# Performance work log

Measured on AMD Instinct MI355X. Metric: run time of the kernel, lower is better.

The kernel has to match this reference:

```python
import jax, jax.numpy as jnp
import numpy as np

EPS = 1e-3


def batchnorm(x, gamma, beta):
    # BatchNorm1d in training mode: batch mean and biased variance over dim 0
    mean = jnp.mean(x, axis=0)
    var = jnp.var(x, axis=0)  # biased, matches torch BN normalization
    return (x - mean) * jax.lax.rsqrt(var + EPS) * gamma + beta


def setup_inputs() -> dict:
    key = jax.random.key(0)
    ks = jax.random.split(key, 12)
    N, C_in, C_out, G = 400000, 64, 128, 30000
    points_xyz = jax.random.normal(ks[0], (N, 3), dtype=jnp.float32) * 10.0
    feat_all = jax.random.normal(ks[1], (N, C_in), dtype=jnp.float32)
    unq_inv = jax.random.randint(ks[2], (N,), 0, G, dtype=jnp.int32)
    s_in = 1.0 / np.sqrt(C_in)
    s3 = 1.0 / np.sqrt(3.0)
    return {
        "points_xyz": points_xyz,
        "feat_all": feat_all,
        "unq_inv": unq_inv,
        "W_pre": jax.random.uniform(ks[3], (C_in, C_out), jnp.float32, -s_in, s_in),
        "b_pre": jax.random.uniform(ks[4], (C_out,), jnp.float32, -s_in, s_in),
        "g1": jnp.ones((C_out,), jnp.float32),
        "be1": jnp.zeros((C_out,), jnp.float32),
        "Wp1": jax.random.uniform(ks[5], (3, C_out), jnp.float32, -s3, s3),
        "bp1": jax.random.uniform(ks[6], (C_out,), jnp.float32, -s3, s3),
        "Wp2": jax.random.uniform(ks[7], (3, C_out), jnp.float32, -s3, s3),
        "bp2": jax.random.uniform(ks[8], (C_out,), jnp.float32, -s3, s3),
        "g2": jnp.ones((C_out,), jnp.float32),
        "be2": jnp.zeros((C_out,), jnp.float32),
        "num_segments": 30000,
    }


def reference(points_xyz, feat_all, unq_inv, W_pre, b_pre, g1, be1,
              Wp1, bp1, Wp2, bp2, g2, be2, num_segments):
    p = jnp.floor(points_xyz)                       # [N, 3]
    feat = batchnorm(feat_all @ W_pre + b_pre, g1, be1)  # [N, C_out]
    pw1 = p @ Wp1 + bp1                             # [N, C_out]
    pw2 = p @ Wp2 + bp2                             # [N, C_out]
    feat_weight = pw1 * feat                        # [N, C_out]
    feat_add = jax.ops.segment_sum(feat_weight, unq_inv,
                                   num_segments=num_segments)  # [G, C_out]
    feat_add = feat_add[unq_inv]                    # gather back: [N, C_out]
    out = pw2 * feat - feat_add
    out = jax.nn.relu(batchnorm(out, g2, be2))
    return out
```

## Files before the change

kernel.cpp:

```cpp
#include <hip/hip_runtime.h>
#include <hip/hip_bf16.h>

typedef unsigned int u32;
typedef unsigned short u16;
typedef __attribute__((ext_vector_type(8))) short short8;
typedef __attribute__((ext_vector_type(4))) float floatx4;

#define COUT 128
#define GSEG 30000
#define BN_EPS 1e-3f

__device__ __forceinline__ u32 f2bf(float x) {
    u32 u = __float_as_uint(x);
    return (u + 0x7fffu + ((u >> 16) & 1u)) >> 16;
}
__device__ __forceinline__ float bf2f(u32 b) { return __uint_as_float(b << 16); }

__device__ __forceinline__ void unpack8(uint4 v, float* f) {
    f[0] = __uint_as_float(v.x << 16); f[1] = __uint_as_float(v.x & 0xffff0000u);
    f[2] = __uint_as_float(v.y << 16); f[3] = __uint_as_float(v.y & 0xffff0000u);
    f[4] = __uint_as_float(v.z << 16); f[5] = __uint_as_float(v.z & 0xffff0000u);
    f[6] = __uint_as_float(v.w << 16); f[7] = __uint_as_float(v.w & 0xffff0000u);
}

__global__ __launch_bounds__(512) void k_prep_w(
    const float* __restrict__ W, u16* __restrict__ wt_hi, u16* __restrict__ wt_lo)
{
    int t = threadIdx.x;
    for (int f = t; f < 8192; f += 512) {
        int k = f >> 7, c = f & 127;
        float w = W[f];
        u32 hb = f2bf(w);
        float lo = w - bf2f(hb);
        wt_hi[c * 64 + k] = (u16)hb;
        wt_lo[c * 64 + k] = (u16)f2bf(lo);
    }
}

__global__ __launch_bounds__(512) void k_gemm_bn1(
    const float* __restrict__ A, const u16* __restrict__ wt_hi, const u16* __restrict__ wt_lo,
    const float* __restrict__ bias, const int* __restrict__ unq, int* __restrict__ cnt,
    u16* __restrict__ lin, float* __restrict__ sum1, float* __restrict__ sumsq1, int n)
{
    __shared__ u16 pack[128 * 136];
    __shared__ float sSum[128], sSq[128];

    const int t = threadIdx.x;
    const int row0 = blockIdx.x * 128;
    if (t < 128) { sSum[t] = 0.f; sSq[t] = 0.f; }

    if (t < 128 && row0 + t < n) atomicAdd(&cnt[unq[row0 + t]], 1);

    const int lane = t & 63, wv = t >> 6;
    const int r = lane & 15, q = lane >> 4;
    const int rw0 = wv * 16;
    const int row_a = row0 + rw0 + r;
    const bool ok = row_a < n;

    short8 arh[2], arl[2];
    const float* ap = A + (size_t)row_a * 64;
#pragma unroll
    for (int ks = 0; ks < 2; ks++) {
        float4 v0 = make_float4(0.f, 0.f, 0.f, 0.f), v1 = v0;
        if (ok) {
            v0 = *(const float4*)(ap + ks * 32 + q * 8);
            v1 = *(const float4*)(ap + ks * 32 + q * 8 + 4);
        }
        float vv[8] = {v0.x, v0.y, v0.z, v0.w, v1.x, v1.y, v1.z, v1.w};
#pragma unroll
        for (int i = 0; i < 8; i++) {
            u32 hb = f2bf(vv[i]);
            float lo = vv[i] - bf2f(hb);
            arh[ks][i] = (short)(u16)hb;
            arl[ks][i] = (short)(u16)f2bf(lo);
        }
    }

    floatx4 acc[8];
#pragma unroll
    for (int ct = 0; ct < 8; ct++) acc[ct] = (floatx4){0.f, 0.f, 0.f, 0.f};

#pragma unroll
    for (int ct = 0; ct < 8; ct++) {
        const u16* whp = wt_hi + (ct * 16 + r) * 64 + q * 8;
        const u16* wlp = wt_lo + (ct * 16 + r) * 64 + q * 8;
#pragma unroll
        for (int ks = 0; ks < 2; ks++) {
            short8 wh = *(const short8*)(whp + ks * 32);
            short8 wl = *(const short8*)(wlp + ks * 32);
            acc[ct] = __builtin_amdgcn_mfma_f32_16x16x32_bf16(arh[ks], wh, acc[ct], 0, 0, 0);
            acc[ct] = __builtin_amdgcn_mfma_f32_16x16x32_bf16(arl[ks], wh, acc[ct], 0, 0, 0);
            acc[ct] = __builtin_amdgcn_mfma_f32_16x16x32_bf16(arh[ks], wl, acc[ct], 0, 0, 0);
        }
    }
    __syncthreads();

#pragma unroll
    for (int ct = 0; ct < 8; ct++) {
        int c = ct * 16 + r;
        float bv = bias[c];
        float ssum = 0.f, ssq = 0.f;
#pragma unroll
        for (int i = 0; i < 4; i++) {
            int lrow = rw0 + q * 4 + i;
            float v = acc[ct][i] + bv;
            if (row0 + lrow >= n) v = 0.f;
            ssum += v; ssq += v * v;
            pack[lrow * 136 + c] = (u16)f2bf(v);
        }
        ssum += __shfl_xor(ssum, 16, 64); ssq += __shfl_xor(ssq, 16, 64);
        ssum += __shfl_xor(ssum, 32, 64); ssq += __shfl_xor(ssq, 32, 64);
        if (lane < 16) { atomicAdd(&sSum[c], ssum); atomicAdd(&sSq[c], ssq); }
    }
    __syncthreads();

#pragma unroll
    for (int j = 0; j < 4; j++) {
        int f = t + j * 512;
        int row = f >> 4, c0 = (f & 15) << 3;
        if (row0 + row < n) {
            uint4 v = *(const uint4*)&pack[row * 136 + c0];
            *(uint4*)(lin + (size_t)(row0 + row) * 128 + c0) = v;
        }
    }
    if (t < 128) { atomicAdd(&sum1[t], sSum[t]); atomicAdd(&sumsq1[t], sSq[t]); }
}

__global__ void k_fin(const float* __restrict__ sum, const float* __restrict__ sumsq,
                      const float* __restrict__ g, const float* __restrict__ be,
                      float* __restrict__ scale, float* __restrict__ shift, float inv_n)
{
    int c = threadIdx.x;
    float mean = sum[c] * inv_n;
    float var = sumsq[c] * inv_n - mean * mean;
    float sc = g[c] * rsqrtf(var + BN_EPS);
    scale[c] = sc;
    shift[c] = be[c] - mean * sc;
}

__global__ __launch_bounds__(1024) void k_scan(const int* __restrict__ cnt,
                                               int* __restrict__ offs,
                                               int* __restrict__ cursor)
{
    __shared__ int wsum[16];
    int t = threadIdx.x, lane = t & 63, wv = t >> 6;
    int base = t * 32;
    int v[32];
    int s = 0;
    if (base + 32 <= GSEG) {
        const int4* cp = (const int4*)(cnt + base);
#pragma unroll
        for (int j = 0; j < 8; j++) {
            int4 q = cp[j];
            v[j * 4 + 0] = q.x; v[j * 4 + 1] = q.y; v[j * 4 + 2] = q.z; v[j * 4 + 3] = q.w;
            s += q.x + q.y + q.z + q.w;
        }
    } else {
#pragma unroll
        for (int j = 0; j < 32; j++) {
            int idx = base + j;
            int x = (idx < GSEG) ? cnt[idx] : 0;
            v[j] = x; s += x;
        }
    }
    int x = s;
#pragma unroll
    for (int d = 1; d < 64; d <<= 1) {
        int u = __shfl_up(x, d, 64);
        if (lane >= d) x += u;
    }
    if (lane == 63) wsum[wv] = x;
    __syncthreads();
    if (t < 16) {
        int w = wsum[t];
#pragma unroll
        for (int d = 1; d < 16; d <<= 1) {
            int u = __shfl_up(w, d, 16);
            if (t >= d) w += u;
        }
        wsum[t] = w;
    }
    __syncthreads();
    int run = (wv ? wsum[wv - 1] : 0) + (x - s);
#pragma unroll
    for (int j = 0; j < 32; j++) {
        int idx = base + j;
        if (idx < GSEG) { offs[idx] = run; cursor[idx] = run; }
        run += v[j];
    }
    if (t == 1023) offs[GSEG] = wsum[15];
}

__global__ __launch_bounds__(256) void k_scatter_idx(const int* __restrict__ unq,
                                                     int* __restrict__ cursor,
                                                     int* __restrict__ order, int n)
{
    int i = blockIdx.x * 256 + threadIdx.x;
    if (i < n) {
        int pos = atomicAdd(&cursor[unq[i]], 1);
        order[pos] = i;
    }
}

__global__ __launch_bounds__(256) void k_segsum(
    const u16* __restrict__ lin, const float* __restrict__ xyz,
    const int* __restrict__ order, const int* __restrict__ offs,
    const float* __restrict__ scale1, const float* __restrict__ shift1,
    const float* __restrict__ Wp1, const float* __restrict__ bp1,
    const float* __restrict__ Wp2, const float* __restrict__ bp2,
    float* __restrict__ feat_add, float* __restrict__ sum2, float* __restrict__ sumsq2,
    int nseg)
{
    __shared__ float sSum[128], sSq[128];
    const int t = threadIdx.x;
    if (t < 128) { sSum[t] = 0.f; sSq[t] = 0.f; }
    __syncthreads();
    const int wave = t >> 6, lane = t & 63;
    const int c = lane * 2;
    const float wa0x = Wp1[c],     wa0y = Wp1[128 + c],     wa0z = Wp1[256 + c],     ba0 = bp1[c];
    const float wa1x = Wp1[c + 1], wa1y = Wp1[128 + c + 1], wa1z = Wp1[256 + c + 1], ba1 = bp1[c + 1];
    const float wb0x = Wp2[c],     wb0y = Wp2[128 + c],     wb0z = Wp2[256 + c],     bb0 = bp2[c];
    const float wb1x = Wp2[c + 1], wb1y = Wp2[128 + c + 1], wb1z = Wp2[256 + c + 1], bb1 = bp2[c + 1];
    const float sc0 = scale1[c], sh0 = shift1[c];
    const float sc1 = scale1[c + 1], sh1 = shift1[c + 1];
    float rs0 = 0.f, rs1 = 0.f, rq0 = 0.f, rq1 = 0.f;
    const int stride = gridDim.x * 4;
    for (int s = blockIdx.x * 4 + wave; s < nseg; s += stride) {
        const int beg = offs[s], end = offs[s + 1];
        const int m = end - beg;
        int rowv = 0; float fxv = 0.f, fyv = 0.f, fzv = 0.f;
        if (lane < m) {
            rowv = order[beg + lane];
            fxv = floorf(xyz[rowv * 3]);
            fyv = floorf(xyz[rowv * 3 + 1]);
            fzv = floorf(xyz[rowv * 3 + 2]);
        }
        float acc0 = 0.f, acc1 = 0.f, p10 = 0.f, p11 = 0.f, p20 = 0.f, p21 = 0.f;
        const int mm = m < 64 ? m : 64;
        for (int j = 0; j < mm; j++) {
            int row = __shfl(rowv, j, 64);
            float px = __shfl(fxv, j, 64);
            float py = __shfl(fyv, j, 64);
            float pz = __shfl(fzv, j, 64);
            u32 l2 = *(const u32*)(lin + (size_t)row * 128 + c);
            float fe0 = fmaf(__uint_as_float(l2 << 16), sc0, sh0);
            float fe1 = fmaf(__uint_as_float(l2 & 0xffff0000u), sc1, sh1);
            float pa0 = fmaf(px, wa0x, fmaf(py, wa0y, fmaf(pz, wa0z, ba0)));
            float pa1 = fmaf(px, wa1x, fmaf(py, wa1y, fmaf(pz, wa1z, ba1)));
            float pb0 = fmaf(px, wb0x, fmaf(py, wb0y, fmaf(pz, wb0z, bb0)));
            float pb1 = fmaf(px, wb1x, fmaf(py, wb1y, fmaf(pz, wb1z, bb1)));
            acc0 = fmaf(pa0, fe0, acc0);
            acc1 = fmaf(pa1, fe1, acc1);
            float t0 = pb0 * fe0, t1 = pb1 * fe1;
            p10 += t0; p11 += t1;
            p20 = fmaf(t0, t0, p20); p21 = fmaf(t1, t1, p21);
        }
        for (int j = 64; j < m; j++) {
            int row = order[beg + j];
            float px = floorf(xyz[row * 3]);
            float py = floorf(xyz[row * 3 + 1]);
            float pz = floorf(xyz[row * 3 + 2]);
            u32 l2 = *(const u32*)(lin + (size_t)row * 128 + c);
            float fe0 = fmaf(__uint_as_float(l2 << 16), sc0, sh0);
            float fe1 = fmaf(__uint_as_float(l2 & 0xffff0000u), sc1, sh1);
            float pa0 = fmaf(px, wa0x, fmaf(py, wa0y, fmaf(pz, wa0z, ba0)));
            float pa1 = fmaf(px, wa1x, fmaf(py, wa1y, fmaf(pz, wa1z, ba1)));
            float pb0 = fmaf(px, wb0x, fmaf(py, wb0y, fmaf(pz, wb0z, bb0)));
            float pb1 = fmaf(px, wb1x, fmaf(py, wb1y, fmaf(pz, wb1z, bb1)));
            acc0 = fmaf(pa0, fe0, acc0);
            acc1 = fmaf(pa1, fe1, acc1);
            float t0 = pb0 * fe0, t1 = pb1 * fe1;
            p10 += t0; p11 += t1;
            p20 = fmaf(t0, t0, p20); p21 = fmaf(t1, t1, p21);
        }
        float2 st; st.x = acc0; st.y = acc1;
        *(float2*)(feat_add + (size_t)s * 128 + c) = st;
        float fm = (float)m;
        rs0 += p10 - fm * acc0;
        rs1 += p11 - fm * acc1;
        rq0 += fmaf(fm * acc0, acc0, p20 - 2.f * acc0 * p10);
        rq1 += fmaf(fm * acc1, acc1, p21 - 2.f * acc1 * p11);
    }
    atomicAdd(&sSum[c], rs0); atomicAdd(&sSum[c + 1], rs1);
    atomicAdd(&sSq[c], rq0);  atomicAdd(&sSq[c + 1], rq1);
    __syncthreads();
    if (t < 128) { atomicAdd(&sum2[t], sSum[t]); atomicAdd(&sumsq2[t], sSq[t]); }
}

__global__ __launch_bounds__(256) void k_final(
    const u16* __restrict__ lin, const float* __restrict__ xyz, const int* __restrict__ unq,
    const float* __restrict__ scale1, const float* __restrict__ shift1,
    const float* __restrict__ Wp2, const float* __restrict__ bp2,
    const float* __restrict__ feat_add,
    const float* __restrict__ scale2, const float* __restrict__ shift2,
    float* __restrict__ out, int n)
{
    __shared__ float sS[128], sH[128], sW3[384], sB[128], sS2[128], sH2[128];
    int t = threadIdx.x;
    if (t < 128) {
        sS[t] = scale1[t]; sH[t] = shift1[t]; sB[t] = bp2[t];
        sW3[t] = Wp2[t]; sW3[128 + t] = Wp2[128 + t]; sW3[256 + t] = Wp2[256 + t];
        sS2[t] = scale2[t]; sH2[t] = shift2[t];
    }
    __syncthreads();
    int row = blockIdx.x * 16 + (t >> 4);
    if (row >= n) return;
    int c0 = (t & 15) * 8;
    uint4 l8 = *(const uint4*)(lin + (size_t)row * 128 + c0);
    float f[8];
    unpack8(l8, f);
    float px = floorf(xyz[row * 3 + 0]);
    float py = floorf(xyz[row * 3 + 1]);
    float pz = floorf(xyz[row * 3 + 2]);
    int g = unq[row];
    const float4* fa = (const float4*)(feat_add + (size_t)g * 128 + c0);
    float4 fa0 = fa[0], fa1 = fa[1];
    float fav[8] = {fa0.x, fa0.y, fa0.z, fa0.w, fa1.x, fa1.y, fa1.z, fa1.w};
    float o[8];
#pragma unroll
    for (int j = 0; j < 8; j++) {
        int c = c0 + j;
        float fe = fmaf(f[j], sS[c], sH[c]);
        float pw = fmaf(px, sW3[c], fmaf(py, sW3[128 + c], fmaf(pz, sW3[256 + c], sB[c])));
        float v = pw * fe - fav[j];
        v = fmaf(v, sS2[c], sH2[c]);
        o[j] = v > 0.f ? v : 0.f;
    }
    float4 s0, s1;
    s0.x = o[0]; s0.y = o[1]; s0.z = o[2]; s0.w = o[3];
    s1.x = o[4]; s1.y = o[5]; s1.z = o[6]; s1.w = o[7];
    float* op = out + (size_t)row * 128 + c0;
    *(float4*)op = s0;
    *(float4*)(op + 4) = s1;
}

extern "C" void kernel_launch(void* const* d_in, const int* in_sizes, int n_in,
                              void* d_out, int out_size, void* d_ws, size_t ws_size,
                              hipStream_t stream)
{
    const float* xyz      = (const float*)d_in[0];
    const float* feat_all = (const float*)d_in[1];
    const int*   unq      = (const int*)d_in[2];
    const float* W_pre    = (const float*)d_in[3];
    const float* b_pre    = (const float*)d_in[4];
    const float* g1       = (const float*)d_in[5];
    const float* be1      = (const float*)d_in[6];
    const float* Wp1      = (const float*)d_in[7];
    const float* bp1      = (const float*)d_in[8];
    const float* Wp2      = (const float*)d_in[9];
    const float* bp2      = (const float*)d_in[10];
    const float* g2       = (const float*)d_in[11];
    const float* be2      = (const float*)d_in[12];
    (void)n_in; (void)out_size; (void)ws_size;

    const int n = in_sizes[0] / 3;

    char* ws = (char*)d_ws;
    float* stats  = (float*)ws;
    float* sum1   = stats;       float* sumsq1 = stats + 128;
    float* sum2   = stats + 256; float* sumsq2 = stats + 384;
    float* scale1 = stats + 512; float* shift1 = stats + 640;
    float* scale2 = stats + 768; float* shift2 = stats + 896;
    int*   cnt      = (int*)(ws + 4096);
    int*   offs     = (int*)(ws + 124160);
    int*   cursor   = (int*)(ws + 244224);
    int*   order    = (int*)(ws + 364288);
    u16*   wt_hi    = (u16*)(ws + 1964544 - 32768);
    u16*   wt_lo    = (u16*)(ws + 1964544 - 16384);
    float* feat_add = (float*)(ws + 1964544);
    u16*   lin      = (u16*)(ws + 17324544);

    hipMemsetAsync(d_ws, 0, 124160, stream);

    k_prep_w<<<1, 512, 0, stream>>>(W_pre, wt_hi, wt_lo);
    k_gemm_bn1<<<(n + 127) / 128, 512, 0, stream>>>(feat_all, wt_hi, wt_lo, b_pre, unq, cnt,
                                                    lin, sum1, sumsq1, n);
    k_fin<<<1, 128, 0, stream>>>(sum1, sumsq1, g1, be1, scale1, shift1, 1.0f / n);

    k_scan<<<1, 1024, 0, stream>>>(cnt, offs, cursor);
    k_scatter_idx<<<(n + 255) / 256, 256, 0, stream>>>(unq, cursor, order, n);
    k_segsum<<<1876, 256, 0, stream>>>(lin, xyz, order, offs, scale1, shift1,
                                       Wp1, bp1, Wp2, bp2, feat_add, sum2, sumsq2, GSEG);
    k_fin<<<1, 128, 0, stream>>>(sum2, sumsq2, g2, be2, scale2, shift2, 1.0f / n);
    k_final<<<(n + 15) / 16, 256, 0, stream>>>(lin, xyz, unq, scale1, shift1, Wp2, bp2,
                                               feat_add, scale2, shift2, (float*)d_out, n);
}
```

Baseline: 614.2 us.

## Pre-swizzle GEMM weights into MFMA fragment order and stage them in LDS

The weight prep kernel now writes the bf16 hi/lo weight splits in per-lane MFMA fragment order. Each GEMM block copies them with coalesced 16-byte loads into LDS that is unioned with the output pack buffer, then reads the fragments from LDS. The A-row loads are issued before the weight copy so their latency overlaps it. This replaces the scattered per-wave global weight reads with one coalesced copy per block, at the cost of an extra barrier and 32KB of LDS traffic per block.

```diff
diff --git a/kernel.cpp b/kernel.cpp
--- a/kernel.cpp
+++ b/kernel.cpp
@@ -24,25 +24,31 @@
 }
 
 __global__ __launch_bounds__(512) void k_prep_w(
-    const float* __restrict__ W, u16* __restrict__ wt_hi, u16* __restrict__ wt_lo)
+    const float* __restrict__ W, u16* __restrict__ wt_f)
 {
     int t = threadIdx.x;
     for (int f = t; f < 8192; f += 512) {
-        int k = f >> 7, c = f & 127;
-        float w = W[f];
+        int ch = f >> 3, e = f & 7;
+        int ct = ch >> 7, ks = (ch >> 6) & 1, lane = ch & 63;
+        int c = ct * 16 + (lane & 15);
+        int k = ks * 32 + (lane >> 4) * 8 + e;
+        float w = W[k * 128 + c];
         u32 hb = f2bf(w);
         float lo = w - bf2f(hb);
-        wt_hi[c * 64 + k] = (u16)hb;
-        wt_lo[c * 64 + k] = (u16)f2bf(lo);
+        wt_f[f] = (u16)hb;
+        wt_f[8192 + f] = (u16)f2bf(lo);
     }
 }
 
 __global__ __launch_bounds__(512) void k_gemm_bn1(
-    const float* __restrict__ A, const u16* __restrict__ wt_hi, const u16* __restrict__ wt_lo,
+    const float* __restrict__ A, const u16* __restrict__ wt_f,
     const float* __restrict__ bias, const int* __restrict__ unq, int* __restrict__ cnt,
     u16* __restrict__ lin, float* __restrict__ sum1, float* __restrict__ sumsq1, int n)
 {
-    __shared__ u16 pack[128 * 136];
+    __shared__ union {
+        u16 w[16384];
+        u16 pack[128 * 136];
+    } sm;
     __shared__ float sSum[128], sSq[128];
 
     const int t = threadIdx.x;
@@ -57,16 +63,26 @@
     const int row_a = row0 + rw0 + r;
     const bool ok = row_a < n;
 
+    const float* ap = A + (size_t)row_a * 64;
+    float4 av[4];
+#pragma unroll
+    for (int ks = 0; ks < 2; ks++) {
+        av[ks * 2]     = ok ? *(const float4*)(ap + ks * 32 + q * 8)     : make_float4(0.f, 0.f, 0.f, 0.f);
+        av[ks * 2 + 1] = ok ? *(const float4*)(ap + ks * 32 + q * 8 + 4) : make_float4(0.f, 0.f, 0.f, 0.f);
+    }
+
+#pragma unroll
+    for (int j = 0; j < 4; j++) {
+        int chunk = j * 512 + t;
+        uint4 v = *(const uint4*)(wt_f + chunk * 8);
+        *(uint4*)&sm.w[chunk * 8] = v;
+    }
+
     short8 arh[2], arl[2];
-    const float* ap = A + (size_t)row_a * 64;
 #pragma unroll
     for (int ks = 0; ks < 2; ks++) {
-        float4 v0 = make_float4(0.f, 0.f, 0.f, 0.f), v1 = v0;
-        if (ok) {
-            v0 = *(const float4*)(ap + ks * 32 + q * 8);
-            v1 = *(const float4*)(ap + ks * 32 + q * 8 + 4);
-        }
-        float vv[8] = {v0.x, v0.y, v0.z, v0.w, v1.x, v1.y, v1.z, v1.w};
+        float vv[8] = {av[ks * 2].x, av[ks * 2].y, av[ks * 2].z, av[ks * 2].w,
+                       av[ks * 2 + 1].x, av[ks * 2 + 1].y, av[ks * 2 + 1].z, av[ks * 2 + 1].w};
 #pragma unroll
         for (int i = 0; i < 8; i++) {
             u32 hb = f2bf(vv[i]);
@@ -80,14 +96,16 @@
 #pragma unroll
     for (int ct = 0; ct < 8; ct++) acc[ct] = (floatx4){0.f, 0.f, 0.f, 0.f};
 
+    __syncthreads();
+
+    const int fbase = lane * 8;
 #pragma unroll
     for (int ct = 0; ct < 8; ct++) {
-        const u16* whp = wt_hi + (ct * 16 + r) * 64 + q * 8;
-        const u16* wlp = wt_lo + (ct * 16 + r) * 64 + q * 8;
 #pragma unroll
         for (int ks = 0; ks < 2; ks++) {
-            short8 wh = *(const short8*)(whp + ks * 32);
-            short8 wl = *(const short8*)(wlp + ks * 32);
+            int fo = (ct * 2 + ks) * 512 + fbase;
+            short8 wh = *(const short8*)&sm.w[fo];
+            short8 wl = *(const short8*)&sm.w[8192 + fo];
             acc[ct] = __builtin_amdgcn_mfma_f32_16x16x32_bf16(arh[ks], wh, acc[ct], 0, 0, 0);
             acc[ct] = __builtin_amdgcn_mfma_f32_16x16x32_bf16(arl[ks], wh, acc[ct], 0, 0, 0);
             acc[ct] = __builtin_amdgcn_mfma_f32_16x16x32_bf16(arh[ks], wl, acc[ct], 0, 0, 0);
@@ -106,7 +124,7 @@
             float v = acc[ct][i] + bv;
             if (row0 + lrow >= n) v = 0.f;
             ssum += v; ssq += v * v;
-            pack[lrow * 136 + c] = (u16)f2bf(v);
+            sm.pack[lrow * 136 + c] = (u16)f2bf(v);
         }
         ssum += __shfl_xor(ssum, 16, 64); ssq += __shfl_xor(ssq, 16, 64);
         ssum += __shfl_xor(ssum, 32, 64); ssq += __shfl_xor(ssq, 32, 64);
@@ -119,7 +137,7 @@
         int f = t + j * 512;
         int row = f >> 4, c0 = (f & 15) << 3;
         if (row0 + row < n) {
-            uint4 v = *(const uint4*)&pack[row * 136 + c0];
+            uint4 v = *(const uint4*)&sm.pack[row * 136 + c0];
             *(uint4*)(lin + (size_t)(row0 + row) * 128 + c0) = v;
         }
     }
@@ -365,15 +383,14 @@
     int*   offs     = (int*)(ws + 124160);
     int*   cursor   = (int*)(ws + 244224);
     int*   order    = (int*)(ws + 364288);
-    u16*   wt_hi    = (u16*)(ws + 1964544 - 32768);
-    u16*   wt_lo    = (u16*)(ws + 1964544 - 16384);
+    u16*   wt_f     = (u16*)(ws + 1964544 - 32768);
     float* feat_add = (float*)(ws + 1964544);
     u16*   lin      = (u16*)(ws + 17324544);
 
     hipMemsetAsync(d_ws, 0, 124160, stream);
 
-    k_prep_w<<<1, 512, 0, stream>>>(W_pre, wt_hi, wt_lo);
-    k_gemm_bn1<<<(n + 127) / 128, 512, 0, stream>>>(feat_all, wt_hi, wt_lo, b_pre, unq, cnt,
+    k_prep_w<<<1, 512, 0, stream>>>(W_pre, wt_f);
+    k_gemm_bn1<<<(n + 127) / 128, 512, 0, stream>>>(feat_all, wt_f, b_pre, unq, cnt,
                                                     lin, sum1, sumsq1, n);
     k_fin<<<1, 128, 0, stream>>>(sum1, sumsq1, g1, be1, scale1, shift1, 1.0f / n);
 
```

Measured after the change: 553.1 us. 10.0% less time.
